# Kernel tuning notes

Measured on AMD Instinct MI355X. Metric: run time of the kernel, lower is better.

The kernel has to match this reference:

```python
import jax, jax.numpy as jnp
import numpy as np

KERNEL_MUL = 2.0
KERNEL_NUM = 5


def _cross_entropy(logits, labels):
    logp = jax.nn.log_softmax(logits, axis=-1)
    return -jnp.take_along_axis(logp, labels[:, None], axis=-1).mean()


def _distill_loss(teacher_logits, student_logits):
    t = jax.nn.softmax(teacher_logits, axis=-1)
    return jnp.sum(-t * jax.nn.log_softmax(student_logits, axis=-1), axis=-1).mean()


def _mk_mmd(source, target):
    # Multi-kernel Gaussian MMD (standard DAN-style implementation).
    ns = source.shape[0]
    total = jnp.concatenate([source, target], axis=0)  # [ns+nt, D]
    sq = jnp.sum(total * total, axis=1)
    l2 = sq[:, None] + sq[None, :] - 2.0 * (total @ total.T)  # [n, n]
    n = total.shape[0]
    bandwidth = jnp.sum(l2) / (n * n - n)
    bandwidth = bandwidth / (KERNEL_MUL ** (KERNEL_NUM // 2))
    kernels = jnp.zeros_like(l2)
    for i in range(KERNEL_NUM):
        kernels = kernels + jnp.exp(-l2 / (bandwidth * (KERNEL_MUL ** i)))
    xx = kernels[:ns, :ns]
    yy = kernels[ns:, ns:]
    xy = kernels[:ns, ns:]
    yx = kernels[ns:, :ns]
    return jnp.mean(xx + yy - xy - yx)


def setup_inputs() -> dict:
    key = jax.random.key(0)
    k1, k2, k3, k4, k5 = jax.random.split(key, 5)
    Ns, Nt, D, C = 4096, 4096, 256, 6
    return {
        "source_feature": jax.random.normal(k1, (Ns, D), dtype=jnp.float32),
        "target_feature": jax.random.normal(k2, (Nt, D), dtype=jnp.float32),
        "source_clf": jax.random.normal(k3, (Ns, C), dtype=jnp.float32),
        "target_clf": jax.random.normal(k4, (Nt, C), dtype=jnp.float32),
        "source_label": jax.random.randint(k5, (Ns,), 0, C, dtype=jnp.int64),
    }


def reference(source_feature, target_feature, source_clf, target_clf, source_label):
    clf_loss = _cross_entropy(source_clf, source_label)

    # Pairwise euclidean distance [Ns, Nt] (cdist, p=2)
    ss = jnp.sum(source_feature * source_feature, axis=1)
    tt = jnp.sum(target_feature * target_feature, axis=1)
    d2 = ss[:, None] + tt[None, :] - 2.0 * (source_feature @ target_feature.T)
    dist = jnp.sqrt(jnp.maximum(d2, 0.0))

    min_idx = jnp.argmin(dist, axis=1)    # nearest target for each source
    min_idx_t = jnp.argmin(dist, axis=0)  # nearest source for each target

    dis_loss = _distill_loss(source_clf, target_clf[min_idx, :])
    dis_loss = dis_loss + _distill_loss(source_clf[min_idx_t, :], target_clf)

    transfer_loss = _mk_mmd(source_feature, target_feature)
    return jnp.stack([clf_loss, dis_loss, transfer_loss])
```

## Files before the change

### kernel.cpp

```cpp
#include <hip/hip_runtime.h>
#include <hip/hip_bf16.h>


#define NS 4096
#define D  256
#define C  6

typedef unsigned long long ull;
typedef unsigned short u16;
typedef __attribute__((ext_vector_type(8))) short short8;
typedef __attribute__((ext_vector_type(4))) unsigned short ushort4v;
typedef __attribute__((ext_vector_type(4))) float floatx4;

#define EXP2F(x) __builtin_amdgcn_exp2f(x)

#define GLD_LDS16(g, l)                                                        \
    __builtin_amdgcn_global_load_lds(                                          \
        (const __attribute__((address_space(1))) unsigned int*)(g),            \
        (__attribute__((address_space(3))) unsigned int*)(l), 16, 0, 0)

__device__ inline u16 f2bf(float f) {
    unsigned u = __float_as_uint(f);
    return (u16)((u + 0x7FFFu + ((u >> 16) & 1u)) >> 16);
}
__device__ inline ull umin64(ull a, ull b) { return a < b ? a : b; }

__global__ __launch_bounds__(256) void kA(const float* __restrict__ src,
                                          const float* __restrict__ tgt,
                                          u16* __restrict__ sb, u16* __restrict__ tb,
                                          float* __restrict__ sq,
                                          ull* __restrict__ rowkey,
                                          ull* __restrict__ colkey,
                                          float* __restrict__ colp) {
    __shared__ float cs[4 * 256];
    int b = blockIdx.x, t = threadIdx.x;
    int w = t >> 6, l = t & 63;
    int r = b * 4 + w;
    const float* row = (r < NS) ? src + (size_t)r * D : tgt + (size_t)(r - NS) * D;
    u16* orow        = (r < NS) ? sb + (size_t)r * D : tb + (size_t)(r - NS) * D;
    float4 v = *(const float4*)&row[l * 4];
    ushort4v o;
    o.x = f2bf(v.x); o.y = f2bf(v.y); o.z = f2bf(v.z); o.w = f2bf(v.w);
    *(ushort4v*)&orow[l * 4] = o;
    float s = v.x * v.x + v.y * v.y + v.z * v.z + v.w * v.w;
    #pragma unroll
    for (int off = 32; off; off >>= 1) s += __shfl_down(s, off, 64);
    if (l == 0) sq[r] = s;

    cs[w * 256 + 4 * l + 0] = v.x;
    cs[w * 256 + 4 * l + 1] = v.y;
    cs[w * 256 + 4 * l + 2] = v.z;
    cs[w * 256 + 4 * l + 3] = v.w;
    __syncthreads();
    float p = cs[t] + cs[256 + t] + cs[512 + t] + cs[768 + t];
    atomicAdd(&colp[(b & 15) * 256 + t], p);

    int gid = b * 256 + t;
    if (gid < NS) rowkey[gid] = ~0ULL;
    else if (gid < 2 * NS) colkey[gid - NS] = ~0ULL;
}

__global__ __launch_bounds__(256) void kB(const float* __restrict__ sq,
                                          const float* __restrict__ colp,
                                          float* __restrict__ bwp) {
    __shared__ float redA[256], redB[256];
    int t = threadIdx.x;
    float ssq = 0.f;
    for (int r = t; r < 2 * NS; r += 256) ssq += sq[r];
    float c = 0.f;
    #pragma unroll
    for (int k = 0; k < 16; k++) c += colp[k * 256 + t];
    redA[t] = ssq;
    redB[t] = c * c;
    __syncthreads();
    for (int off = 128; off; off >>= 1) {
        if (t < off) { redA[t] += redA[t + off]; redB[t] += redB[t + off]; }
        __syncthreads();
    }
    if (t == 0) {
        double n = 2.0 * NS;
        double sum_l2 = 2.0 * n * (double)redA[0] - 2.0 * (double)redB[0];
        bwp[0] = (float)(sum_l2 / (n * n - n) / 4.0);
    }
}

__global__ __launch_bounds__(256, 3) void k3_mfma(const u16* __restrict__ Sb,
                                                  const u16* __restrict__ Tb,
                                                  const float* __restrict__ sq,
                                                  const float* __restrict__ bwp,
                                                  double* __restrict__ accD,
                                                  ull* __restrict__ rowkey,
                                                  ull* __restrict__ colkey) {
    int bz = blockIdx.z;
    int ti = blockIdx.y, tj = blockIdx.x;
    if (bz != 0 && ti > tj) return;

    const u16* Am = (bz == 2) ? Tb : Sb;
    const u16* Bm = (bz == 1) ? Sb : Tb;
    const float* sqA = (bz == 2) ? sq + NS : sq;
    const float* sqB = (bz == 1) ? sq : sq + NS;
    int zacc = (bz == 0) ? 2 : (bz - 1);

    __shared__ __align__(16) u16 Atile[128 * 64];
    __shared__ __align__(16) u16 Btile[128 * 64];
    __shared__ float sqa_s[128], sqb_s[128];
    __shared__ ull rminL[128], cminL[128];
    __shared__ float wsum[4];

    int tid = threadIdx.x;
    int w = tid >> 6, ln = tid & 63;
    int wm = w >> 1, wn = w & 1;
    int quad = ln >> 4, lrow = ln & 15;
    int row0 = ti * 128, col0 = tj * 128;

    if (tid < 128) { sqa_s[tid] = sqA[row0 + tid]; rminL[tid] = ~0ULL; }
    else           { sqb_s[tid - 128] = sqB[col0 + tid - 128]; cminL[tid - 128] = ~0ULL; }

    int lr8 = ln >> 3;
    int cg  = (ln & 7) ^ lr8;

    floatx4 acc[4][4] = {};

    #pragma unroll 2
    for (int kc = 0; kc < D; kc += 64) {
        #pragma unroll
        for (int i = 0; i < 4; i++) {
            int lrb = w * 32 + i * 8;
            GLD_LDS16(Am + (size_t)(row0 + lrb + lr8) * D + kc + cg * 8,
                      &Atile[lrb * 64]);
            GLD_LDS16(Bm + (size_t)(col0 + lrb + lr8) * D + kc + cg * 8,
                      &Btile[lrb * 64]);
        }
        __syncthreads();
        #pragma unroll
        for (int ks = 0; ks < 2; ks++) {
            short8 af[4], bf4[4];
            #pragma unroll
            for (int rf = 0; rf < 4; rf++) {
                int rl = wm * 64 + rf * 16 + lrow;
                int ch = (ks * 4 + quad) ^ (lrow & 7);
                af[rf] = *(const short8*)&Atile[rl * 64 + ch * 8];
            }
            #pragma unroll
            for (int cf = 0; cf < 4; cf++) {
                int rl = wn * 64 + cf * 16 + lrow;
                int ch = (ks * 4 + quad) ^ (lrow & 7);
                bf4[cf] = *(const short8*)&Btile[rl * 64 + ch * 8];
            }
            #pragma unroll
            for (int rf = 0; rf < 4; rf++)
                #pragma unroll
                for (int cf = 0; cf < 4; cf++)
                    acc[rf][cf] = __builtin_amdgcn_mfma_f32_16x16x32_bf16(
                        af[rf], bf4[cf], acc[rf][cf], 0, 0, 0);
        }
        __syncthreads();
    }

    float sb_c[4];
    #pragma unroll
    for (int cf = 0; cf < 4; cf++)
        sb_c[cf] = sqb_s[wn * 64 + cf * 16 + lrow];

    float nlog = -1.4426950408889634f / (bwp[0] * 16.0f);

    int rbase = row0 + wm * 64, cbase = col0 + wn * 64;
    float tsum = 0.f;

    if (bz == 0) {
        ull ck[4];
        #pragma unroll
        for (int cf = 0; cf < 4; cf++) ck[cf] = ~0ULL;
        #pragma unroll
        for (int rf = 0; rf < 4; rf++) {
            float sa4[4];
            #pragma unroll
            for (int reg = 0; reg < 4; reg++)
                sa4[reg] = sqa_s[wm * 64 + rf * 16 + quad * 4 + reg];
            ull rk[4];
            #pragma unroll
            for (int reg = 0; reg < 4; reg++) rk[reg] = ~0ULL;
            #pragma unroll
            for (int cf = 0; cf < 4; cf++) {
                int gj = cbase + cf * 16 + lrow;
                float sbv = sb_c[cf];
                #pragma unroll
                for (int reg = 0; reg < 4; reg++) {
                    int gi = rbase + rf * 16 + quad * 4 + reg;
                    float l2 = sa4[reg] + sbv - 2.0f * acc[rf][cf][reg];
                    float t4 = EXP2F(l2 * nlog);
                    float t3 = t4 * t4, t2 = t3 * t3, t1 = t2 * t2, t0 = t1 * t1;
                    tsum += t0 + t1 + t2 + t3 + t4;
                    ull bits = ((ull)__float_as_uint(fmaxf(l2, 0.f))) << 32;
                    rk[reg] = umin64(rk[reg], bits | (unsigned)gj);
                    ck[cf]  = umin64(ck[cf],  bits | (unsigned)gi);
                }
            }
            #pragma unroll
            for (int reg = 0; reg < 4; reg++) {
                ull v = rk[reg];
                #pragma unroll
                for (int m = 1; m <= 8; m <<= 1)
                    v = umin64(v, (ull)__shfl_xor((unsigned long long)v, m, 64));
                if (lrow == 0)
                    atomicMin(&rminL[wm * 64 + rf * 16 + quad * 4 + reg], v);
            }
        }
        #pragma unroll
        for (int cf = 0; cf < 4; cf++) {
            ull v = ck[cf];
            v = umin64(v, (ull)__shfl_xor((unsigned long long)v, 16, 64));
            v = umin64(v, (ull)__shfl_xor((unsigned long long)v, 32, 64));
            if (quad == 0)
                atomicMin(&cminL[wn * 64 + cf * 16 + lrow], v);
        }
    } else {
        #pragma unroll
        for (int rf = 0; rf < 4; rf++) {
            float sa4[4];
            #pragma unroll
            for (int reg = 0; reg < 4; reg++)
                sa4[reg] = sqa_s[wm * 64 + rf * 16 + quad * 4 + reg];
            #pragma unroll
            for (int cf = 0; cf < 4; cf++) {
                int gj = cbase + cf * 16 + lrow;
                float sbv = sb_c[cf];
                #pragma unroll
                for (int reg = 0; reg < 4; reg++) {
                    int gi = rbase + rf * 16 + quad * 4 + reg;
                    float l2 = sa4[reg] + sbv - 2.0f * acc[rf][cf][reg];
                    float t4 = EXP2F(l2 * nlog);
                    float t3 = t4 * t4, t2 = t3 * t3, t1 = t2 * t2, t0 = t1 * t1;
                    if (ti < tj || gi < gj)
                        tsum += t0 + t1 + t2 + t3 + t4;
                }
            }
        }
    }

    #pragma unroll
    for (int off = 32; off; off >>= 1) tsum += __shfl_down(tsum, off, 64);
    if (ln == 0) wsum[w] = tsum;
    __syncthreads();
    if (tid == 0)
        atomicAdd(&accD[zacc], (double)(wsum[0] + wsum[1] + wsum[2] + wsum[3]));
    if (bz == 0) {
        if (tid < 128) atomicMin(&rowkey[row0 + tid], rminL[tid]);
        else           atomicMin(&colkey[col0 + tid - 128], cminL[tid - 128]);
    }
}

__global__ __launch_bounds__(256) void k4(const float* __restrict__ sclf,
                                          const float* __restrict__ tclf,
                                          const int* __restrict__ label,
                                          const ull* __restrict__ rowkey,
                                          const ull* __restrict__ colkey,
                                          double* __restrict__ accD,
                                          int* __restrict__ cnts,
                                          float* __restrict__ out) {
    int i = blockIdx.x * 256 + threadIdx.x;
    float clf, dis = 0.f;

    const float* x = sclf + (size_t)i * C;
    float mx = x[0];
    #pragma unroll
    for (int c = 1; c < C; c++) mx = fmaxf(mx, x[c]);
    float sx = 0.f;
    #pragma unroll
    for (int c = 0; c < C; c++) sx += __expf(x[c] - mx);
    clf = mx + __logf(sx) - x[label[i]];

    {
        int j = (int)(rowkey[i] & 0xffffffffULL);
        const float* y = tclf + (size_t)j * C;
        float my = y[0];
        #pragma unroll
        for (int c = 1; c < C; c++) my = fmaxf(my, y[c]);
        float sy = 0.f;
        #pragma unroll
        for (int c = 0; c < C; c++) sy += __expf(y[c] - my);
        float dot = 0.f;
        #pragma unroll
        for (int c = 0; c < C; c++) dot += __expf(x[c] - mx) * y[c];
        dis += my + __logf(sy) - dot / sx;
    }
    {
        int it = (int)(colkey[i] & 0xffffffffULL);
        const float* xt = sclf + (size_t)it * C;
        float mt = xt[0];
        #pragma unroll
        for (int c = 1; c < C; c++) mt = fmaxf(mt, xt[c]);
        float st = 0.f;
        #pragma unroll
        for (int c = 0; c < C; c++) st += __expf(xt[c] - mt);
        const float* zz = tclf + (size_t)i * C;
        float mz = zz[0];
        #pragma unroll
        for (int c = 1; c < C; c++) mz = fmaxf(mz, zz[c]);
        float sz = 0.f;
        #pragma unroll
        for (int c = 0; c < C; c++) sz += __expf(zz[c] - mz);
        float dot2 = 0.f;
        #pragma unroll
        for (int c = 0; c < C; c++) dot2 += __expf(xt[c] - mt) * zz[c];
        dis += mz + __logf(sz) - dot2 / st;
    }

    #pragma unroll
    for (int off = 32; off; off >>= 1) {
        clf += __shfl_down(clf, off, 64);
        dis += __shfl_down(dis, off, 64);
    }
    if ((threadIdx.x & 63) == 0) {
        atomicAdd(&accD[3], (double)clf);
        atomicAdd(&accD[4], (double)dis);
    }
    __threadfence();
    __shared__ int isLast;
    if (threadIdx.x == 0) isLast = (atomicAdd(&cnts[0], 1) == (int)gridDim.x - 1);
    __syncthreads();
    if (isLast && threadIdx.x == 0) {
        double Sxx  = atomicAdd(&accD[0], 0.0);
        double Syy  = atomicAdd(&accD[1], 0.0);
        double Sxy  = atomicAdd(&accD[2], 0.0);
        double clfS = atomicAdd(&accD[3], 0.0);
        double disS = atomicAdd(&accD[4], 0.0);
        double ns = (double)NS;
        out[0] = (float)(clfS / ns);
        out[1] = (float)(disS / ns);
        double sum_xx = 2.0 * Sxx + ns * 5.0;
        double sum_yy = 2.0 * Syy + ns * 5.0;
        out[2] = (float)((sum_xx + sum_yy - 2.0 * Sxy) / (ns * ns));
    }
}

extern "C" void kernel_launch(void* const* d_in, const int* in_sizes, int n_in,
                              void* d_out, int out_size, void* d_ws, size_t ws_size,
                              hipStream_t stream) {
    const float* src  = (const float*)d_in[0];
    const float* tgt  = (const float*)d_in[1];
    const float* sclf = (const float*)d_in[2];
    const float* tclf = (const float*)d_in[3];
    const int*   lab  = (const int*)d_in[4];
    float* out = (float*)d_out;

    char* ws = (char*)d_ws;
    u16* sb     = (u16*)ws;
    u16* tb     = sb + (size_t)NS * D;
    ull* rowkey = (ull*)(ws + 2 * (size_t)NS * D * 2);
    ull* colkey = rowkey + NS;
    float* sq   = (float*)(colkey + NS);
    float* bwp  = sq + 2 * NS;
    char* zb    = (char*)bwp + 64;
    double* accD = (double*)zb;
    int* cnts    = (int*)(zb + 64);
    float* colp  = (float*)(zb + 128);
    size_t zbytes = 128 + 16 * 256 * 4;

    hipMemsetAsync(zb, 0, zbytes, stream);
    kA<<<2048, 256, 0, stream>>>(src, tgt, sb, tb, sq, rowkey, colkey, colp);
    kB<<<1, 256, 0, stream>>>(sq, colp, bwp);
    k3_mfma<<<dim3(32, 32, 3), 256, 0, stream>>>(sb, tb, sq, bwp, accD, rowkey, colkey);
    k4<<<16, 256, 0, stream>>>(sclf, tclf, lab, rowkey, colkey, accD, cnts, out);
}
```

Baseline: 138.9 us.

## Launch only needed triangular tiles via 1D grid, raise occupancy, split finalization kernel

The 3D grid that launched 3072 blocks, a third of them returning immediately for the lower-triangle tiles of the symmetric xx/yy blocks, is replaced by a compact 1D grid of 2080 blocks. Each block decodes its (bz, ti, tj) with a triangular-index formula, which removes the empty block launches. Launch bounds go from 3 to 4 waves per SIMD, which may pressure registers. The last-block detection with a counter and threadfence in k4 is replaced by a separate one-thread finalization kernel, adding one launch.

```diff
diff --git a/kernel.cpp b/kernel.cpp
--- a/kernel.cpp
+++ b/kernel.cpp
@@ -84,16 +84,27 @@
     }
 }
 
-__global__ __launch_bounds__(256, 3) void k3_mfma(const u16* __restrict__ Sb,
+__global__ __launch_bounds__(256, 4) void k3_mfma(const u16* __restrict__ Sb,
                                                   const u16* __restrict__ Tb,
                                                   const float* __restrict__ sq,
                                                   const float* __restrict__ bwp,
                                                   double* __restrict__ accD,
                                                   ull* __restrict__ rowkey,
                                                   ull* __restrict__ colkey) {
-    int bz = blockIdx.z;
-    int ti = blockIdx.y, tj = blockIdx.x;
-    if (bz != 0 && ti > tj) return;
+    int idx = blockIdx.x;
+    int bz, ti, tj;
+    if (idx < 1024) {
+        bz = 0; ti = idx >> 5; tj = idx & 31;
+    } else {
+        int t = idx - 1024;
+        bz = 1;
+        if (t >= 528) { t -= 528; bz = 2; }
+        int i = (int)((65.0f - sqrtf(4225.0f - 8.0f * (float)t)) * 0.5f);
+        if ((i + 1) * (64 - i) / 2 <= t) i++;
+        else if (i * (65 - i) / 2 > t) i--;
+        ti = i;
+        tj = i + (t - i * (65 - i) / 2);
+    }
 
     const u16* Am = (bz == 2) ? Tb : Sb;
     const u16* Bm = (bz == 1) ? Sb : Tb;
@@ -255,9 +266,7 @@
                                           const int* __restrict__ label,
                                           const ull* __restrict__ rowkey,
                                           const ull* __restrict__ colkey,
-                                          double* __restrict__ accD,
-                                          int* __restrict__ cnts,
-                                          float* __restrict__ out) {
+                                          double* __restrict__ accD) {
     int i = blockIdx.x * 256 + threadIdx.x;
     float clf, dis = 0.f;
 
@@ -315,23 +324,16 @@
         atomicAdd(&accD[3], (double)clf);
         atomicAdd(&accD[4], (double)dis);
     }
-    __threadfence();
-    __shared__ int isLast;
-    if (threadIdx.x == 0) isLast = (atomicAdd(&cnts[0], 1) == (int)gridDim.x - 1);
-    __syncthreads();
-    if (isLast && threadIdx.x == 0) {
-        double Sxx  = atomicAdd(&accD[0], 0.0);
-        double Syy  = atomicAdd(&accD[1], 0.0);
-        double Sxy  = atomicAdd(&accD[2], 0.0);
-        double clfS = atomicAdd(&accD[3], 0.0);
-        double disS = atomicAdd(&accD[4], 0.0);
-        double ns = (double)NS;
-        out[0] = (float)(clfS / ns);
-        out[1] = (float)(disS / ns);
-        double sum_xx = 2.0 * Sxx + ns * 5.0;
-        double sum_yy = 2.0 * Syy + ns * 5.0;
-        out[2] = (float)((sum_xx + sum_yy - 2.0 * Sxy) / (ns * ns));
-    }
+}
+
+__global__ void k5(const double* __restrict__ accD, float* __restrict__ out) {
+    double Sxx = accD[0], Syy = accD[1], Sxy = accD[2];
+    double ns = (double)NS;
+    out[0] = (float)(accD[3] / ns);
+    out[1] = (float)(accD[4] / ns);
+    double sum_xx = 2.0 * Sxx + ns * 5.0;
+    double sum_yy = 2.0 * Syy + ns * 5.0;
+    out[2] = (float)((sum_xx + sum_yy - 2.0 * Sxy) / (ns * ns));
 }
 
 extern "C" void kernel_launch(void* const* d_in, const int* in_sizes, int n_in,
@@ -353,13 +355,13 @@
     float* bwp  = sq + 2 * NS;
     char* zb    = (char*)bwp + 64;
     double* accD = (double*)zb;
-    int* cnts    = (int*)(zb + 64);
-    float* colp  = (float*)(zb + 128);
-    size_t zbytes = 128 + 16 * 256 * 4;
+    float* colp  = (float*)(zb + 64);
+    size_t zbytes = 64 + 16 * 256 * 4;
 
     hipMemsetAsync(zb, 0, zbytes, stream);
     kA<<<2048, 256, 0, stream>>>(src, tgt, sb, tb, sq, rowkey, colkey, colp);
     kB<<<1, 256, 0, stream>>>(sq, colp, bwp);
-    k3_mfma<<<dim3(32, 32, 3), 256, 0, stream>>>(sb, tb, sq, bwp, accD, rowkey, colkey);
-    k4<<<16, 256, 0, stream>>>(sclf, tclf, lab, rowkey, colkey, accD, cnts, out);
-}
+    k3_mfma<<<2080, 256, 0, stream>>>(sb, tb, sq, bwp, accD, rowkey, colkey);
+    k4<<<16, 256, 0, stream>>>(sclf, tclf, lab, rowkey, colkey, accD);
+    k5<<<1, 1, 0, stream>>>(accD, out);
+}
```

After: 172.3 us. 1.24x slower.
